# Kernel tuning notes

Measured on AMD Instinct MI355X. Metric: run time of the kernel, lower is better.

## Reference

```python
import jax, jax.numpy as jnp
import numpy as np
from jax import lax

KS = 3
N = KS * KS


def _conv(x, W, b, pad, stride):
    out = lax.conv_general_dilated(
        x, W, window_strides=(stride, stride),
        padding=[(pad, pad), (pad, pad)],
        dimension_numbers=("NCHW", "OIHW", "NCHW"))
    return out + b[None, :, None, None]


def setup_inputs() -> dict:
    key = jax.random.key(0)
    ks = jax.random.split(key, 5)
    b, c, h, w, outc = 16, 64, 64, 64, 128
    return {
        "x": jax.random.normal(ks[0], (b, c, h, w), jnp.float32),
        "W_off": jax.random.normal(ks[1], (2 * N, c, KS, KS), jnp.float32) * 0.05,
        "b_off": jax.random.normal(ks[2], (2 * N,), jnp.float32) * 0.05,
        "W_k": jax.random.normal(ks[3], (outc, c, KS, KS), jnp.float32) * 0.05,
        "b_k": jax.random.normal(ks[4], (outc,), jnp.float32) * 0.05,
    }


def _deform_conv(x, W_off, b_off, W_k, b_k):
    b, c, h, w = x.shape
    offset = _conv(x, W_off, b_off, pad=1, stride=1)  # [b, 2N, h, w]

    # kernel-grid offsets, flattened with x (row) index first: n = i*ks + j
    rng = jnp.arange(KS, dtype=x.dtype) - (KS - 1) // 2  # [-1, 0, 1]
    pnx = jnp.repeat(rng, KS)  # [N]
    pny = jnp.tile(rng, KS)    # [N]

    # sampling positions p = p0 + p_n + offset, clamped into the image
    px = jnp.arange(h, dtype=x.dtype)[None, None, :, None] + pnx[None, :, None, None] + offset[:, :N]
    py = jnp.arange(w, dtype=x.dtype)[None, None, None, :] + pny[None, :, None, None] + offset[:, N:]
    px = jnp.clip(px, 0, h - 1)
    py = jnp.clip(py, 0, w - 1)

    fx = jnp.floor(px)
    fy = jnp.floor(py)
    tx = px - fx  # fractional parts (bilinear weights)
    ty = py - fy
    x0 = fx.astype(jnp.int32)
    y0 = fy.astype(jnp.int32)
    x1 = jnp.minimum(x0 + 1, h - 1)  # out-of-range tap carries zero weight
    y1 = jnp.minimum(y0 + 1, w - 1)

    x_hw = x.transpose(0, 2, 3, 1).reshape(b, h * w, c)  # [b, hw, c]

    def gather(ix, iy):
        idx = (ix * w + iy).reshape(b, -1, 1)  # [b, N*h*w, 1]
        return jnp.take_along_axis(x_hw, idx, axis=1).reshape(b, N, h, w, c)

    wx0, wx1 = (1 - tx)[..., None], tx[..., None]
    wy0, wy1 = (1 - ty)[..., None], ty[..., None]
    # 4-tap bilinear interpolation == the original's sparse G @ x
    xo = (gather(x0, y0) * wx0 * wy0 + gather(x1, y0) * wx1 * wy0
          + gather(x0, y1) * wx0 * wy1 + gather(x1, y1) * wx1 * wy1)  # [b,N,h,w,c]

    # _reshape_x_offset: out[b,c, i_h*ks+i, i_w*ks+j] = xo[b, i*ks+j, i_h, i_w, c]
    xo = xo.reshape(b, KS, KS, h, w, c).transpose(0, 5, 3, 1, 4, 2)
    xo = xo.reshape(b, c, h * KS, w * KS)

    return _conv(xo, W_k, b_k, pad=0, stride=KS)  # [b, outc, h, w]


def reference(x, W_off, b_off, W_k, b_k):
    return _deform_conv(x, W_off, b_off, W_k, b_k)
```

## Files before the change

### kernel.cpp

```cpp
#include <hip/hip_runtime.h>

typedef __attribute__((ext_vector_type(8))) short bf16x8;
typedef __attribute__((ext_vector_type(4))) float floatx4;

__device__ __forceinline__ unsigned short f2bf(float f) {
    unsigned int u = __float_as_uint(f);
    u += 0x7FFFu + ((u >> 16) & 1u);
    return (unsigned short)(u >> 16);
}

__global__ __launch_bounds__(256) void prep_all(const float* __restrict__ x,
        const float* __restrict__ Wk, const float* __restrict__ Woff,
        unsigned short* __restrict__ xt, unsigned short* __restrict__ Wkb,
        float* __restrict__ Wofft) {
    int bb = blockIdx.x;
    if (bb < 1024) {
        __shared__ float tile[64][65];
        int b = bb >> 6, y = bb & 63;
        const float* src = x + (size_t)b * 262144 + y * 64;
        int tx = threadIdx.x & 15, tg = threadIdx.x >> 4;
#pragma unroll
        for (int i = 0; i < 4; i++) {
            int c = tg + i * 16;
            float4 v = *(const float4*)(src + (size_t)c * 4096 + tx * 4);
            tile[c][tx * 4 + 0] = v.x; tile[c][tx * 4 + 1] = v.y;
            tile[c][tx * 4 + 2] = v.z; tile[c][tx * 4 + 3] = v.w;
        }
        __syncthreads();
        unsigned short* dst = xt + (size_t)bb * 4096;
#pragma unroll
        for (int i = 0; i < 4; i++) {
            int xc = tg + i * 16;
            int c4 = tx * 4;
            ushort4 v;
            v.x = f2bf(tile[c4 + 0][xc]); v.y = f2bf(tile[c4 + 1][xc]);
            v.z = f2bf(tile[c4 + 2][xc]); v.w = f2bf(tile[c4 + 3][xc]);
            *(ushort4*)(dst + xc * 64 + c4) = v;
        }
    } else if (bb < 1312) {
        int idx = (bb - 1024) * 256 + threadIdx.x;
        int c = idx & 63;
        int rest = idx >> 6;
        int oc = rest & 127;
        int tap = rest >> 7;
        Wkb[idx] = f2bf(Wk[(oc * 64 + c) * 9 + tap]);
    } else {
        int idx = (bb - 1312) * 256 + threadIdx.x;
        if (idx < 10368) {
            int n = idx % 18;
            int ct = idx / 18;
            int t = ct % 9;
            int cin = ct / 9;
            Wofft[idx] = Woff[(n * 64 + cin) * 9 + t];
        }
    }
}

__global__ __launch_bounds__(256) void offset_kernel(const float* __restrict__ x,
        const float* __restrict__ Wofft, const float* __restrict__ boff,
        float* __restrict__ off) {
    __shared__ float xs[4][1600];
    int tid = threadIdx.x;
    int lane = tid & 63;
    int wgrp = __builtin_amdgcn_readfirstlane(tid >> 6);
    int py = lane >> 3, pxl = lane & 7;
    int tileX = blockIdx.x * 8, tileY = blockIdx.y * 8;
    int b = blockIdx.z;
    const float* xc0 = x + (size_t)(b * 64 + wgrp * 16) * 4096;
    for (int i = lane; i < 1600; i += 64) {
        int c = i / 100, rem = i - c * 100;
        int iy = rem / 10, ix = rem - iy * 10;
        int gy = tileY + iy - 1, gx = tileX + ix - 1;
        float v = 0.f;
        if (gy >= 0 && gy < 64 && gx >= 0 && gx < 64)
            v = xc0[c * 4096 + gy * 64 + gx];
        xs[wgrp][i] = v;
    }
    __syncthreads();
    float acc[18];
#pragma unroll
    for (int n = 0; n < 18; n++) acc[n] = 0.f;
    const float* wbase = Wofft + wgrp * (16 * 162);
    for (int c = 0; c < 16; c++) {
        const float* wc = wbase + c * 162;
        const float* xb = &xs[wgrp][c * 100 + py * 10 + pxl];
#pragma unroll
        for (int t = 0; t < 9; t++) {
            float xv = xb[(t / 3) * 10 + (t % 3)];
#pragma unroll
            for (int n = 0; n < 18; n++)
                acc[n] = fmaf(xv, wc[t * 18 + n], acc[n]);
        }
    }
    __syncthreads();
    float* red = &xs[0][0];
    if (wgrp) {
#pragma unroll
        for (int n = 0; n < 18; n++)
            red[((wgrp - 1) * 64 + lane) * 18 + n] = acc[n];
    }
    __syncthreads();
    if (wgrp == 0) {
        int gyx = (tileY + py) * 64 + tileX + pxl;
        float* ob = off + (size_t)b * 73728 + gyx;
#pragma unroll
        for (int n = 0; n < 18; n++) {
            float v = acc[n] + red[lane * 18 + n] + red[(64 + lane) * 18 + n]
                    + red[(128 + lane) * 18 + n] + boff[n];
            ob[n << 12] = v;
        }
    }
}

__global__ __launch_bounds__(256, 4) void fused_kernel(
        const unsigned short* __restrict__ xt,
        const float* __restrict__ off,
        const unsigned short* __restrict__ Wkb,
        const float* __restrict__ bias,
        float* __restrict__ out) {
    __shared__ unsigned short As[128 * 72];
    int tid = threadIdx.x;
    int wave = tid >> 6, lane = tid & 63;
    int frow = lane & 15, quad = lane >> 4;
    int bb = blockIdx.x;
    int xcd = bb & 7, idx = bb >> 3;
    int b = xcd * 2 + (idx >> 6);
    int pxBase = (idx & 63) * 64;
    int px = pxBase + wave * 16 + frow;
    const char* img = (const char*)(xt + (size_t)b * 262144) + quad * 16;
    const float* offb = off + (size_t)b * 73728;

    floatx4 acc[8];
#pragma unroll
    for (int i = 0; i < 8; i++) acc[i] = (floatx4)(0.f);

    int fk = quad * 8;
    int y = px >> 6, xx = px & 63;

    for (int tap = 0; tap < 9; tap++) {
        __syncthreads();
        {
            int oc = tid >> 1, seg = (tid & 1) * 32;
            const unsigned short* srcw = Wkb + tap * 8192 + oc * 64 + seg;
            unsigned short* dstw = As + oc * 72 + seg;
#pragma unroll
            for (int i = 0; i < 4; i++)
                *(bf16x8*)(dstw + i * 8) = *(const bf16x8*)(srcw + i * 8);
        }
        __syncthreads();
        float orow = offb[tap * 4096 + px];
        float ocol = offb[(9 + tap) * 4096 + px];
        float pr = (float)(y + tap / 3 - 1) + orow;
        float pc = (float)(xx + tap % 3 - 1) + ocol;
        pr = fminf(fmaxf(pr, 0.f), 63.f);
        pc = fminf(fmaxf(pc, 0.f), 63.f);
        float fr = floorf(pr), fc = floorf(pc);
        float tr = pr - fr, tc = pc - fc;
        int r0 = (int)fr, c0 = (int)fc;
        int r1 = min(r0 + 1, 63), c1 = min(c0 + 1, 63);
        float w00 = (1.f - tr) * (1.f - tc);
        float w01 = (1.f - tr) * tc;
        float w10 = tr * (1.f - tc);
        float w11 = tr * tc;
        int o00 = (r0 * 64 + c0) * 128;
        int o01 = (r0 * 64 + c1) * 128;
        int o10 = (r1 * 64 + c0) * 128;
        int o11 = (r1 * 64 + c1) * 128;

        bf16x8 bfrag[2];
#pragma unroll
        for (int kc = 0; kc < 2; kc++) {
            int4 u00 = __builtin_bit_cast(int4, *(const bf16x8*)(img + o00 + kc * 64));
            int4 u01 = __builtin_bit_cast(int4, *(const bf16x8*)(img + o01 + kc * 64));
            int4 u10 = __builtin_bit_cast(int4, *(const bf16x8*)(img + o10 + kc * 64));
            int4 u11 = __builtin_bit_cast(int4, *(const bf16x8*)(img + o11 + kc * 64));
            int4 r;
#pragma unroll
            for (int wd = 0; wd < 4; wd++) {
                int a00 = (wd == 0) ? u00.x : (wd == 1) ? u00.y : (wd == 2) ? u00.z : u00.w;
                int a01 = (wd == 0) ? u01.x : (wd == 1) ? u01.y : (wd == 2) ? u01.z : u01.w;
                int a10 = (wd == 0) ? u10.x : (wd == 1) ? u10.y : (wd == 2) ? u10.z : u10.w;
                int a11 = (wd == 0) ? u11.x : (wd == 1) ? u11.y : (wd == 2) ? u11.z : u11.w;
                float vl = w00 * __uint_as_float((unsigned)a00 << 16)
                         + w01 * __uint_as_float((unsigned)a01 << 16)
                         + w10 * __uint_as_float((unsigned)a10 << 16)
                         + w11 * __uint_as_float((unsigned)a11 << 16);
                float vh = w00 * __uint_as_float((unsigned)a00 & 0xffff0000u)
                         + w01 * __uint_as_float((unsigned)a01 & 0xffff0000u)
                         + w10 * __uint_as_float((unsigned)a10 & 0xffff0000u)
                         + w11 * __uint_as_float((unsigned)a11 & 0xffff0000u);
                unsigned pk = __builtin_amdgcn_perm(
                    __float_as_uint(vh) + 0x8000u,
                    __float_as_uint(vl) + 0x8000u, 0x07060302u);
                if (wd == 0) r.x = (int)pk; else if (wd == 1) r.y = (int)pk;
                else if (wd == 2) r.z = (int)pk; else r.w = (int)pk;
            }
            bfrag[kc] = __builtin_bit_cast(bf16x8, r);
        }
#pragma unroll
        for (int kc = 0; kc < 2; kc++) {
#pragma unroll
            for (int mt = 0; mt < 8; mt++) {
                bf16x8 af = *(const bf16x8*)&As[(mt * 16 + frow) * 72 + kc * 32 + fk];
                acc[mt] = __builtin_amdgcn_mfma_f32_16x16x32_bf16(af, bfrag[kc], acc[mt], 0, 0, 0);
            }
        }
    }

    float* outb = out + (size_t)b * 524288 + px;
#pragma unroll
    for (int mt = 0; mt < 8; mt++) {
#pragma unroll
        for (int rg = 0; rg < 4; rg++) {
            int oc = mt * 16 + quad * 4 + rg;
            outb[oc * 4096] = acc[mt][rg] + bias[oc];
        }
    }
}

extern "C" void kernel_launch(void* const* d_in, const int* in_sizes, int n_in,
                              void* d_out, int out_size, void* d_ws, size_t ws_size,
                              hipStream_t stream) {
    const float* x    = (const float*)d_in[0];
    const float* Woff = (const float*)d_in[1];
    const float* boff = (const float*)d_in[2];
    const float* Wk   = (const float*)d_in[3];
    const float* bk   = (const float*)d_in[4];
    float* out = (float*)d_out;

    char* ws = (char*)d_ws;
    unsigned short* xt  = (unsigned short*)ws;
    float* offb         = (float*)(ws + 8388608);
    unsigned short* Wkb = (unsigned short*)(ws + 13107200);
    float* Wofft        = (float*)(ws + 13254656);

    prep_all<<<1353, 256, 0, stream>>>(x, Wk, Woff, xt, Wkb, Wofft);
    offset_kernel<<<dim3(8, 8, 16), 256, 0, stream>>>(x, Wofft, boff, offb);
    fused_kernel<<<1024, 256, 0, stream>>>(xt, offb, Wkb, bk, out);
}
```

Measured before the change: 158.1 us.

## Fuse offset convolution into main kernel via bf16 MFMA and double-buffer weights

Removes the separate fp32 offset-convolution kernel and instead computes the 18 offset channels inside the fused kernel as an MFMA GEMM over the bf16 channel-last input, storing offsets in shared memory. Weight matrices for both convolutions are pre-packed into MFMA fragment order and double-buffered in LDS with register prefetch, removing one barrier per tap. This eliminates a kernel launch and the global round trip of the offset tensor, at the cost of computing offsets in bf16 precision, which may perturb sampling positions.

```diff
diff --git a/kernel.cpp b/kernel.cpp
--- a/kernel.cpp
+++ b/kernel.cpp
@@ -11,8 +11,8 @@
 
 __global__ __launch_bounds__(256) void prep_all(const float* __restrict__ x,
         const float* __restrict__ Wk, const float* __restrict__ Woff,
-        unsigned short* __restrict__ xt, unsigned short* __restrict__ Wkb,
-        float* __restrict__ Wofft) {
+        unsigned short* __restrict__ xt, unsigned short* __restrict__ Wkb2,
+        unsigned short* __restrict__ Woffb) {
     int bb = blockIdx.x;
     if (bb < 1024) {
         __shared__ float tile[64][65];
@@ -39,86 +39,39 @@
         }
     } else if (bb < 1312) {
         int idx = (bb - 1024) * 256 + threadIdx.x;
-        int c = idx & 63;
-        int rest = idx >> 6;
-        int oc = rest & 127;
-        int tap = rest >> 7;
-        Wkb[idx] = f2bf(Wk[(oc * 64 + c) * 9 + tap]);
+        int tap = idx >> 13;
+        int r = idx & 8191;
+        int tile = r >> 9;
+        int ln = (r >> 3) & 63;
+        int j = r & 7;
+        int mt = tile >> 1, kc = tile & 1;
+        int oc = mt * 16 + (ln & 15);
+        int c = kc * 32 + (ln >> 4) * 8 + j;
+        Wkb2[idx] = f2bf(Wk[(oc * 64 + c) * 9 + tap]);
     } else {
         int idx = (bb - 1312) * 256 + threadIdx.x;
-        if (idx < 10368) {
-            int n = idx % 18;
-            int ct = idx / 18;
-            int t = ct % 9;
-            int cin = ct / 9;
-            Wofft[idx] = Woff[(n * 64 + cin) * 9 + t];
-        }
-    }
-}
-
-__global__ __launch_bounds__(256) void offset_kernel(const float* __restrict__ x,
-        const float* __restrict__ Wofft, const float* __restrict__ boff,
-        float* __restrict__ off) {
-    __shared__ float xs[4][1600];
-    int tid = threadIdx.x;
-    int lane = tid & 63;
-    int wgrp = __builtin_amdgcn_readfirstlane(tid >> 6);
-    int py = lane >> 3, pxl = lane & 7;
-    int tileX = blockIdx.x * 8, tileY = blockIdx.y * 8;
-    int b = blockIdx.z;
-    const float* xc0 = x + (size_t)(b * 64 + wgrp * 16) * 4096;
-    for (int i = lane; i < 1600; i += 64) {
-        int c = i / 100, rem = i - c * 100;
-        int iy = rem / 10, ix = rem - iy * 10;
-        int gy = tileY + iy - 1, gx = tileX + ix - 1;
-        float v = 0.f;
-        if (gy >= 0 && gy < 64 && gx >= 0 && gx < 64)
-            v = xc0[c * 4096 + gy * 64 + gx];
-        xs[wgrp][i] = v;
-    }
-    __syncthreads();
-    float acc[18];
-#pragma unroll
-    for (int n = 0; n < 18; n++) acc[n] = 0.f;
-    const float* wbase = Wofft + wgrp * (16 * 162);
-    for (int c = 0; c < 16; c++) {
-        const float* wc = wbase + c * 162;
-        const float* xb = &xs[wgrp][c * 100 + py * 10 + pxl];
-#pragma unroll
-        for (int t = 0; t < 9; t++) {
-            float xv = xb[(t / 3) * 10 + (t % 3)];
-#pragma unroll
-            for (int n = 0; n < 18; n++)
-                acc[n] = fmaf(xv, wc[t * 18 + n], acc[n]);
-        }
-    }
-    __syncthreads();
-    float* red = &xs[0][0];
-    if (wgrp) {
-#pragma unroll
-        for (int n = 0; n < 18; n++)
-            red[((wgrp - 1) * 64 + lane) * 18 + n] = acc[n];
-    }
-    __syncthreads();
-    if (wgrp == 0) {
-        int gyx = (tileY + py) * 64 + tileX + pxl;
-        float* ob = off + (size_t)b * 73728 + gyx;
-#pragma unroll
-        for (int n = 0; n < 18; n++) {
-            float v = acc[n] + red[lane * 18 + n] + red[(64 + lane) * 18 + n]
-                    + red[(128 + lane) * 18 + n] + boff[n];
-            ob[n << 12] = v;
-        }
+        int tap = idx >> 11;
+        int r = idx & 2047;
+        int tile = r >> 9;
+        int ln = (r >> 3) & 63;
+        int j = r & 7;
+        int mt = tile >> 1, kc = tile & 1;
+        int n = mt * 16 + (ln & 15);
+        int c = kc * 32 + (ln >> 4) * 8 + j;
+        float v = (n < 18) ? Woff[(n * 64 + c) * 9 + tap] : 0.f;
+        Woffb[idx] = f2bf(v);
     }
 }
 
 __global__ __launch_bounds__(256, 4) void fused_kernel(
         const unsigned short* __restrict__ xt,
-        const float* __restrict__ off,
-        const unsigned short* __restrict__ Wkb,
+        const unsigned short* __restrict__ Wkb2,
+        const unsigned short* __restrict__ Woffb,
+        const float* __restrict__ boff,
         const float* __restrict__ bias,
         float* __restrict__ out) {
-    __shared__ unsigned short As[128 * 72];
+    __shared__ unsigned short As[2][8192];
+    __shared__ float offs[64][20];
     int tid = threadIdx.x;
     int wave = tid >> 6, lane = tid & 63;
     int frow = lane & 15, quad = lane >> 4;
@@ -126,30 +79,71 @@
     int xcd = bb & 7, idx = bb >> 3;
     int b = xcd * 2 + (idx >> 6);
     int pxBase = (idx & 63) * 64;
-    int px = pxBase + wave * 16 + frow;
+    int pl = wave * 16 + frow;
+    int px = pxBase + pl;
+    int y = px >> 6, xx = px & 63;
     const char* img = (const char*)(xt + (size_t)b * 262144) + quad * 16;
-    const float* offb = off + (size_t)b * 73728;
+
+    float bv[2][4];
+#pragma unroll
+    for (int mt = 0; mt < 2; mt++)
+#pragma unroll
+        for (int rg = 0; rg < 4; rg++) {
+            int n = mt * 16 + quad * 4 + rg;
+            bv[mt][rg] = (n < 18) ? boff[n] : 0.f;
+        }
+
+    floatx4 acc1[2];
+    acc1[0] = (floatx4)(0.f); acc1[1] = (floatx4)(0.f);
+    bf16x8 aw = *(const bf16x8*)(Woffb + tid * 8);
+    *(bf16x8*)&As[0][tid * 8] = aw;
+    for (int tap = 0; tap < 9; tap++) {
+        if (tap < 8) aw = *(const bf16x8*)(Woffb + (tap + 1) * 2048 + tid * 8);
+        __syncthreads();
+        int ry = y + tap / 3 - 1, rx = xx + tap % 3 - 1;
+        bool valid = (ry >= 0) & (ry < 64) & (rx >= 0) & (rx < 64);
+        const char* src = img + ((ry * 64 + rx) << 7);
+        const unsigned short* abuf = &As[tap & 1][0];
+        bf16x8 bz = {};
+#pragma unroll
+        for (int kc = 0; kc < 2; kc++) {
+            bf16x8 bfr = valid ? *(const bf16x8*)(src + kc * 64) : bz;
+#pragma unroll
+            for (int mt = 0; mt < 2; mt++) {
+                bf16x8 af = *(const bf16x8*)&abuf[(mt * 2 + kc) * 512 + lane * 8];
+                acc1[mt] = __builtin_amdgcn_mfma_f32_16x16x32_bf16(af, bfr, acc1[mt], 0, 0, 0);
+            }
+        }
+        if (tap < 8) *(bf16x8*)&As[(tap + 1) & 1][tid * 8] = aw;
+    }
+#pragma unroll
+    for (int mt = 0; mt < 2; mt++)
+#pragma unroll
+        for (int rg = 0; rg < 4; rg++) {
+            int n = mt * 16 + quad * 4 + rg;
+            if (n < 18) offs[pl][n] = acc1[mt][rg] + bv[mt][rg];
+        }
 
     floatx4 acc[8];
 #pragma unroll
     for (int i = 0; i < 8; i++) acc[i] = (floatx4)(0.f);
-
-    int fk = quad * 8;
-    int y = px >> 6, xx = px & 63;
+    bf16x8 wk[4];
+#pragma unroll
+    for (int i = 0; i < 4; i++)
+        wk[i] = *(const bf16x8*)(Wkb2 + i * 2048 + tid * 8);
+    __syncthreads();
+#pragma unroll
+    for (int i = 0; i < 4; i++)
+        *(bf16x8*)&As[0][i * 2048 + tid * 8] = wk[i];
 
     for (int tap = 0; tap < 9; tap++) {
+        if (tap < 8)
+#pragma unroll
+            for (int i = 0; i < 4; i++)
+                wk[i] = *(const bf16x8*)(Wkb2 + (tap + 1) * 8192 + i * 2048 + tid * 8);
         __syncthreads();
-        {
-            int oc = tid >> 1, seg = (tid & 1) * 32;
-            const unsigned short* srcw = Wkb + tap * 8192 + oc * 64 + seg;
-            unsigned short* dstw = As + oc * 72 + seg;
-#pragma unroll
-            for (int i = 0; i < 4; i++)
-                *(bf16x8*)(dstw + i * 8) = *(const bf16x8*)(srcw + i * 8);
-        }
-        __syncthreads();
-        float orow = offb[tap * 4096 + px];
-        float ocol = offb[(9 + tap) * 4096 + px];
+        float orow = offs[pl][tap];
+        float ocol = offs[pl][9 + tap];
         float pr = (float)(y + tap / 3 - 1) + orow;
         float pc = (float)(xx + tap % 3 - 1) + ocol;
         pr = fminf(fmaxf(pr, 0.f), 63.f);
@@ -197,14 +191,18 @@
             }
             bfrag[kc] = __builtin_bit_cast(bf16x8, r);
         }
-#pragma unroll
-        for (int kc = 0; kc < 2; kc++) {
+        const unsigned short* abuf = &As[tap & 1][0];
+#pragma unroll
+        for (int kc = 0; kc < 2; kc++)
 #pragma unroll
             for (int mt = 0; mt < 8; mt++) {
-                bf16x8 af = *(const bf16x8*)&As[(mt * 16 + frow) * 72 + kc * 32 + fk];
+                bf16x8 af = *(const bf16x8*)&abuf[(mt * 2 + kc) * 512 + lane * 8];
                 acc[mt] = __builtin_amdgcn_mfma_f32_16x16x32_bf16(af, bfrag[kc], acc[mt], 0, 0, 0);
             }
-        }
+        if (tap < 8)
+#pragma unroll
+            for (int i = 0; i < 4; i++)
+                *(bf16x8*)&As[(tap + 1) & 1][i * 2048 + tid * 8] = wk[i];
     }
 
     float* outb = out + (size_t)b * 524288 + px;
@@ -229,12 +227,10 @@
     float* out = (float*)d_out;
 
     char* ws = (char*)d_ws;
-    unsigned short* xt  = (unsigned short*)ws;
-    float* offb         = (float*)(ws + 8388608);
-    unsigned short* Wkb = (unsigned short*)(ws + 13107200);
-    float* Wofft        = (float*)(ws + 13254656);
-
-    prep_all<<<1353, 256, 0, stream>>>(x, Wk, Woff, xt, Wkb, Wofft);
-    offset_kernel<<<dim3(8, 8, 16), 256, 0, stream>>>(x, Wofft, boff, offb);
-    fused_kernel<<<1024, 256, 0, stream>>>(xt, offb, Wkb, bk, out);
-}
+    unsigned short* xt    = (unsigned short*)ws;
+    unsigned short* Wkb2  = (unsigned short*)(ws + 8388608);
+    unsigned short* Woffb = (unsigned short*)(ws + 8536064);
+
+    prep_all<<<1384, 256, 0, stream>>>(x, Wk, Woff, xt, Wkb2, Woffb);
+    fused_kernel<<<1024, 256, 0, stream>>>(xt, Wkb2, Woffb, boff, bk, out);
+}
```

After: 132.3 us. 1.2x faster.
